# Kernel tuning notes

Hardware: AMD Instinct MI355X
Metric: run time of the kernel (lower is better)

Reference implementation:

```python
import jax, jax.numpy as jnp
import numpy as np

NUM_HEADS = 16

def rotate_half(x):
    x1, x2 = jnp.split(x, 2, axis=-1)
    return jnp.concatenate((-x2, x1), axis=-1)

def setup_inputs() -> dict:
    key = jax.random.key(0)
    ks = jax.random.split(key, 5)
    b, n, dim, hd = 2, 2048, 1024, 64
    return {
        "x": jax.random.normal(ks[0], (b, n, dim), dtype=jnp.float32),
        "Wqkv": jax.random.normal(ks[1], (3 * dim, dim), dtype=jnp.float32) * (dim ** -0.5),
        "Wproj": jax.random.normal(ks[2], (dim, dim), dtype=jnp.float32) * (dim ** -0.5),
        "bproj": jnp.zeros((dim,), dtype=jnp.float32),
        "sin": jax.random.normal(ks[3], (n, hd), dtype=jnp.float32),
        "cos": jax.random.normal(ks[4], (n, hd), dtype=jnp.float32),
    }

def reference(x, Wqkv, Wproj, bproj, sin, cos):
    b, n, dim = x.shape
    h = NUM_HEADS
    d = dim // h
    qkv = x @ Wqkv.T
    qkv = qkv.reshape(b, n, 3, h, d).transpose(2, 0, 3, 1, 4)
    q, k, v = qkv[0], qkv[1], qkv[2]
    # RoPE: sin/cos [n, d] broadcast over [b, h, n, d]
    q = q * cos + rotate_half(q) * sin
    k = k * cos + rotate_half(k) * sin
    # SDPA (non-causal, no dropout at eval)
    scale = d ** -0.5
    scores = jnp.einsum("bhnd,bhmd->bhnm", q, k) * scale
    attn = jax.nn.softmax(scores, axis=-1)
    out = jnp.einsum("bhnm,bhmd->bhnd", attn, v)
    # merge heads: [b, h, n, d] -> [b, n, h*d]
    out = out.transpose(0, 2, 1, 3).reshape(b, n, dim)
    return out @ Wproj.T + bproj
```

## Files before the change

kernel.cpp:

```cpp
#include <hip/hip_runtime.h>
#include <hip/hip_fp16.h>

typedef _Float16 f16;
typedef _Float16 half8 __attribute__((ext_vector_type(8)));
typedef _Float16 half4v __attribute__((ext_vector_type(4)));
typedef float f32x4 __attribute__((ext_vector_type(4)));

#define QSCALE 0.18033688011112042f
#define SHIFT2 17.312340490667560f

__device__ __forceinline__ void gload_lds16(const void* g, void* lds) {
  __builtin_amdgcn_global_load_lds(
      (__attribute__((address_space(1))) void*)g,
      (__attribute__((address_space(3))) void*)lds, 16, 0, 0);
}

__global__ __launch_bounds__(256) void cvt_all_kernel(
    const float* __restrict__ x, const float* __restrict__ wqkv,
    const float* __restrict__ wproj, f16* __restrict__ xh,
    f16* __restrict__ wqkvh, f16* __restrict__ wprojh) {
  int i = blockIdx.x * 256 + threadIdx.x;
  const float* src; f16* dst; int off;
  if (i < 1048576)      { src = x;     dst = xh;     off = i; }
  else if (i < 1835008) { src = wqkv;  dst = wqkvh;  off = i - 1048576; }
  else                  { src = wproj; dst = wprojh; off = i - 1835008; }
  float4 v = ((const float4*)src)[off];
  half4v o;
  o.x = (f16)v.x; o.y = (f16)v.y; o.z = (f16)v.z; o.w = (f16)v.w;
  ((half4v*)dst)[off] = o;
}

template<int EPI>
__global__ __launch_bounds__(256) void hgemm_kernel(
    const f16* __restrict__ A16, const f16* __restrict__ B, int K,
    const float* __restrict__ cosT, const float* __restrict__ sinT,
    f16* __restrict__ Qout, f16* __restrict__ Kout, f16* __restrict__ Vtout,
    const float* __restrict__ bias, float* __restrict__ Cout) {
  constexpr int BN = (EPI == 0) ? 128 : 64;
  constexpr int NJ = (EPI == 0) ? 4 : 2;
  __shared__ f16 As[2][128 * 32];
  __shared__ f16 Bs[2][BN * 32];
  const int tid = threadIdx.x;
  const int lane = tid & 63, w = tid >> 6;
  const int fr = lane & 15, fkg = lane >> 4;
  const int wm = (w >> 1) * 64;
  const int wn = (EPI == 0) ? (w & 1) * 64 : (w & 1) * 16;
  const long long rowBase = (long long)blockIdx.x * 128;
  const long long colBase = (long long)blockIdx.y * BN;

  f32x4 acc[4][NJ] = {};
  const f16* Ab = A16 + rowBase * K;
  const f16* Bb = B + colBase * K;

  const int srow = lane >> 2;
  const int kcol = ((lane & 3) ^ ((lane >> 3) & 3)) * 8;
  const int sw = (fkg ^ ((fr >> 1) & 3)) * 8;

  auto stage = [&](int buf, int k0) {
#pragma unroll
    for (int r = 0; r < 2; ++r) {
      int c = r * 4 + w;
      gload_lds16(Ab + (long long)(c * 16 + srow) * K + k0 + kcol, &As[buf][c * 512]);
    }
    if (EPI == 0) {
#pragma unroll
      for (int r = 0; r < 2; ++r) {
        int c = r * 4 + w;
        gload_lds16(Bb + (long long)(c * 16 + srow) * K + k0 + kcol, &Bs[buf][c * 512]);
      }
    } else {
      int c = w;
      gload_lds16(Bb + (long long)(c * 16 + srow) * K + k0 + kcol, &Bs[buf][c * 512]);
    }
  };

  const int NT = K >> 5;
  stage(0, 0);
  stage(1, 32);
  for (int t = 0; t < NT; ++t) {
    const int buf = t & 1;
    const int k0 = t << 5;
    if (t + 1 < NT) {
      if constexpr (EPI == 0) asm volatile("s_waitcnt vmcnt(4)" ::: "memory");
      else                    asm volatile("s_waitcnt vmcnt(3)" ::: "memory");
    } else {
      asm volatile("s_waitcnt vmcnt(0)" ::: "memory");
    }
    __builtin_amdgcn_s_barrier();
    __builtin_amdgcn_sched_barrier(0);
    half8 a[4], b[NJ];
#pragma unroll
    for (int i = 0; i < 4; ++i)
      a[i] = *(const half8*)(&As[buf][((wm >> 4) + i) * 512 + fr * 32 + sw]);
#pragma unroll
    for (int j = 0; j < NJ; ++j) {
      int chunk = (EPI == 0) ? ((wn >> 4) + j) : ((wn >> 4) + j * 2);
      b[j] = *(const half8*)(&Bs[buf][chunk * 512 + fr * 32 + sw]);
    }
    asm volatile("s_waitcnt lgkmcnt(0)" ::: "memory");
    __builtin_amdgcn_sched_barrier(0);
    __builtin_amdgcn_s_barrier();
    if (t + 2 < NT) stage(buf, k0 + 64);
#pragma unroll
    for (int i = 0; i < 4; ++i)
#pragma unroll
      for (int j = 0; j < NJ; ++j)
        acc[i][j] = __builtin_amdgcn_mfma_f32_16x16x32_f16(a[i], b[j], acc[i][j], 0, 0, 0);
  }

  if (EPI == 0) {
#pragma unroll
    for (int i = 0; i < 4; ++i) {
#pragma unroll
      for (int r = 0; r < 4; ++r) {
        int rg = (int)rowBase + wm + i * 16 + fkg * 4 + r;
        int bidx = rg >> 11, nn = rg & 2047;
#pragma unroll
        for (int j = 0; j < 4; ++j) {
          int cg = (int)colBase + wn + j * 16 + fr;
          int t = cg >> 10, cc = cg & 1023;
          int head = cc >> 6, d = cc & 63;
          int bh = bidx * 16 + head;
          float v = acc[i][j][r];
          if (t == 2) {
            Vtout[((long long)bh * 64 + d) * 2048 + nn] = (f16)v;
          } else {
            float pal = acc[i][j ^ 2][r];
            float cs = cosT[nn * 64 + d];
            float sn = sinT[nn * 64 + d];
            v = v * cs + (d < 32 ? -pal : pal) * sn;
            if (t == 0) v *= QSCALE;
            f16 hv = (f16)v;
            if (t == 0) Qout[((long long)bh * 2048 + nn) * 64 + d] = hv;
            else        Kout[((long long)bh * 2048 + nn) * 64 + d] = hv;
          }
        }
      }
    }
  } else {
#pragma unroll
    for (int i = 0; i < 4; ++i)
#pragma unroll
      for (int r = 0; r < 4; ++r) {
        long long rg = rowBase + wm + i * 16 + fkg * 4 + r;
#pragma unroll
        for (int j = 0; j < NJ; ++j) {
          int cg = (int)colBase + wn + j * 32 + fr;
          Cout[rg * 1024 + cg] = acc[i][j][r] + bias[cg];
        }
      }
  }
}

__global__ __launch_bounds__(256) void attn_kernel(
    const f16* __restrict__ Q, const f16* __restrict__ Kb,
    const f16* __restrict__ Vt, f16* __restrict__ Om) {
  __shared__ f16 Ks[2][64 * 64];
  __shared__ f16 Vs[2][64 * 64];
  const int tid = threadIdx.x;
  const int lane = tid & 63, w = tid >> 6;
  const int fr = lane & 15, fkg = lane >> 4, fk = fkg * 8;

  const int lin = blockIdx.x;
  const int slot = lin >> 3;
  const int bh = (lin & 7) * 4 + (slot >> 4);
  const int q0 = (slot & 15) * 128 + w * 32;

  const f16* Kbh = Kb + (long long)bh * 2048 * 64;
  const f16* Vbh = Vt + (long long)bh * 64 * 2048;

  half8 aq[2][2];
#pragma unroll
  for (int m = 0; m < 2; ++m)
#pragma unroll
    for (int ks = 0; ks < 2; ++ks)
      aq[m][ks] = *(const half8*)(Q + ((long long)bh * 2048 + q0 + m * 16 + fr) * 64 +
                                  ks * 32 + fk);

  half8 ones_frag;
#pragma unroll
  for (int j = 0; j < 8; ++j) ones_frag[j] = (fr == 0) ? (f16)1.0f : (f16)0.0f;

  f32x4 acc[2][4] = {};
  f32x4 accL[2] = {};

  const int srow = lane >> 3;
  const int ssub = ((lane & 7) ^ srow) * 8;
  int prow[2];
#pragma unroll
  for (int c = 0; c < 2; ++c) {
    int R = w * 16 + c * 8 + srow;
    prow[c] = (R & 0x23) | ((R & 0x0C) << 1) | ((R & 0x10) >> 2);
  }

  auto stage = [&](int buf, int kv0) {
#pragma unroll
    for (int c = 0; c < 2; ++c) {
      int rb = w * 16 + c * 8;
      gload_lds16(Kbh + (long long)(kv0 + prow[c]) * 64 + ssub,
                  &Ks[buf][rb * 64]);
      gload_lds16(Vbh + (long long)(rb + srow) * 2048 + kv0 + ssub,
                  &Vs[buf][rb * 64]);
    }
  };

  stage(0, 0);
  stage(1, 64);
  for (int t = 0; t < 32; ++t) {
    const int buf = t & 1;
    if (t + 1 < 32) asm volatile("s_waitcnt vmcnt(4)" ::: "memory");
    else            asm volatile("s_waitcnt vmcnt(0)" ::: "memory");
    __builtin_amdgcn_s_barrier();
    __builtin_amdgcn_sched_barrier(0);

    f32x4 z[2][4];
#pragma unroll
    for (int n = 0; n < 4; ++n) {
      half8 bk0 = *(const half8*)(&Ks[buf][(n * 16 + fr) * 64 + ((fkg ^ (fr & 7)) * 8)]);
      half8 bk1 = *(const half8*)(&Ks[buf][(n * 16 + fr) * 64 + (((4 | fkg) ^ (fr & 7)) * 8)]);
#pragma unroll
      for (int m = 0; m < 2; ++m) {
        f32x4 tz = {0.f, 0.f, 0.f, 0.f};
        tz = __builtin_amdgcn_mfma_f32_16x16x32_f16(bk0, aq[m][0], tz, 0, 0, 0);
        tz = __builtin_amdgcn_mfma_f32_16x16x32_f16(bk1, aq[m][1], tz, 0, 0, 0);
        z[m][n] = tz;
      }
    }

    half8 av[2][4];
#pragma unroll
    for (int ks = 0; ks < 2; ++ks)
#pragma unroll
      for (int dd = 0; dd < 4; ++dd)
        av[ks][dd] = *(const half8*)(&Vs[buf][(dd * 16 + fr) * 64 +
                                              ((((ks << 2) | fkg) ^ (fr & 7)) * 8)]);

    half8 ap[2][2];
#pragma unroll
    for (int m = 0; m < 2; ++m)
#pragma unroll
      for (int ks = 0; ks < 2; ++ks)
#pragma unroll
        for (int h = 0; h < 2; ++h)
#pragma unroll
          for (int r = 0; r < 4; ++r)
            ap[m][ks][h * 4 + r] =
                (f16)__builtin_amdgcn_exp2f(z[m][2 * ks + h][r] - SHIFT2);

#pragma unroll
    for (int ks = 0; ks < 2; ++ks) {
#pragma unroll
      for (int m = 0; m < 2; ++m)
        accL[m] = __builtin_amdgcn_mfma_f32_16x16x32_f16(ones_frag, ap[m][ks], accL[m], 0, 0, 0);
#pragma unroll
      for (int dd = 0; dd < 4; ++dd)
#pragma unroll
        for (int m = 0; m < 2; ++m)
          acc[m][dd] = __builtin_amdgcn_mfma_f32_16x16x32_f16(av[ks][dd], ap[m][ks], acc[m][dd], 0, 0, 0);
    }

    asm volatile("s_waitcnt lgkmcnt(0)" ::: "memory");
    __builtin_amdgcn_sched_barrier(0);
    __builtin_amdgcn_s_barrier();
    if (t + 2 < 32) stage(buf, (t + 2) * 64);
  }

  const int b = bh >> 4, h = bh & 15;
#pragma unroll
  for (int m = 0; m < 2; ++m) {
    float l = __shfl(accL[m][0], fr);
    float inv = 1.f / l;
#pragma unroll
    for (int dd = 0; dd < 4; ++dd) {
      half4v o;
#pragma unroll
      for (int r = 0; r < 4; ++r) o[r] = (f16)(acc[m][dd][r] * inv);
      *(half4v*)(&Om[((long long)b * 2048 + q0 + m * 16 + fr) * 1024 +
                     h * 64 + dd * 16 + fkg * 4]) = o;
    }
  }
}

extern "C" void kernel_launch(void* const* d_in, const int* in_sizes, int n_in,
                              void* d_out, int out_size, void* d_ws, size_t ws_size,
                              hipStream_t stream) {
  (void)in_sizes; (void)n_in; (void)out_size; (void)ws_size;
  const float* x     = (const float*)d_in[0];
  const float* Wqkv  = (const float*)d_in[1];
  const float* Wproj = (const float*)d_in[2];
  const float* bproj = (const float*)d_in[3];
  const float* sinT  = (const float*)d_in[4];
  const float* cosT  = (const float*)d_in[5];
  float* out = (float*)d_out;

  f16* ws     = (f16*)d_ws;
  f16* xh     = ws;
  f16* Om     = ws;
  f16* Wqkvh  = ws + 4194304;
  f16* Wprojh = ws + 7340032;
  f16* Qb     = ws + 8388608;
  f16* Kb     = ws + 12582912;
  f16* Vtb    = ws + 16777216;

  cvt_all_kernel<<<8192, 256, 0, stream>>>(x, Wqkv, Wproj, xh, Wqkvh, Wprojh);

  hgemm_kernel<0><<<dim3(32, 24), 256, 0, stream>>>(
      xh, Wqkvh, 1024, cosT, sinT, Qb, Kb, Vtb, nullptr, nullptr);

  attn_kernel<<<512, 256, 0, stream>>>(Qb, Kb, Vtb, Om);

  hgemm_kernel<1><<<dim3(32, 16), 256, 0, stream>>>(
      Om, Wprojh, 1024, nullptr, nullptr, nullptr, nullptr, nullptr, bproj, out);
}
```

Before: 125.9 us.

## Triple-buffer LDS staging in attention and half of QKV GEMM to drop a barrier

Adds a three-buffer LDS pipeline to the attention kernel and to a new GEMM variant. The next-next tile is prefetched right after the single per-iteration barrier, which removes the second barrier and the lgkmcnt wait at the end of each iteration. The QKV projection is now split into two launches over column halves, one using the old double-buffered path and one the new triple-buffered path, which looks like a side-by-side comparison. The cost is more LDS per block, which may lower occupancy, plus one extra kernel launch.

Result: slower. 159.4 us (+26.6%).

```diff
diff --git a/kernel.cpp b/kernel.cpp
--- a/kernel.cpp
+++ b/kernel.cpp
@@ -30,23 +30,24 @@
   ((half4v*)dst)[off] = o;
 }
 
-template<int EPI>
+template<int EPI, int VAR>
 __global__ __launch_bounds__(256) void hgemm_kernel(
-    const f16* __restrict__ A16, const f16* __restrict__ B, int K,
+    const f16* __restrict__ A16, const f16* __restrict__ B, int K, int yoff,
     const float* __restrict__ cosT, const float* __restrict__ sinT,
     f16* __restrict__ Qout, f16* __restrict__ Kout, f16* __restrict__ Vtout,
     const float* __restrict__ bias, float* __restrict__ Cout) {
   constexpr int BN = (EPI == 0) ? 128 : 64;
   constexpr int NJ = (EPI == 0) ? 4 : 2;
-  __shared__ f16 As[2][128 * 32];
-  __shared__ f16 Bs[2][BN * 32];
+  constexpr int NBUF = (VAR == 0) ? 2 : 3;
+  __shared__ f16 As[NBUF][128 * 32];
+  __shared__ f16 Bs[NBUF][BN * 32];
   const int tid = threadIdx.x;
   const int lane = tid & 63, w = tid >> 6;
   const int fr = lane & 15, fkg = lane >> 4;
   const int wm = (w >> 1) * 64;
   const int wn = (EPI == 0) ? (w & 1) * 64 : (w & 1) * 16;
   const long long rowBase = (long long)blockIdx.x * 128;
-  const long long colBase = (long long)blockIdx.y * BN;
+  const long long colBase = (long long)(blockIdx.y + yoff) * BN;
 
   f32x4 acc[4][NJ] = {};
   const f16* Ab = A16 + rowBase * K;
@@ -77,35 +78,66 @@
   const int NT = K >> 5;
   stage(0, 0);
   stage(1, 32);
-  for (int t = 0; t < NT; ++t) {
-    const int buf = t & 1;
-    const int k0 = t << 5;
-    if (t + 1 < NT) {
-      if constexpr (EPI == 0) asm volatile("s_waitcnt vmcnt(4)" ::: "memory");
-      else                    asm volatile("s_waitcnt vmcnt(3)" ::: "memory");
-    } else {
-      asm volatile("s_waitcnt vmcnt(0)" ::: "memory");
-    }
-    __builtin_amdgcn_s_barrier();
-    __builtin_amdgcn_sched_barrier(0);
-    half8 a[4], b[NJ];
-#pragma unroll
-    for (int i = 0; i < 4; ++i)
-      a[i] = *(const half8*)(&As[buf][((wm >> 4) + i) * 512 + fr * 32 + sw]);
-#pragma unroll
-    for (int j = 0; j < NJ; ++j) {
-      int chunk = (EPI == 0) ? ((wn >> 4) + j) : ((wn >> 4) + j * 2);
-      b[j] = *(const half8*)(&Bs[buf][chunk * 512 + fr * 32 + sw]);
-    }
-    asm volatile("s_waitcnt lgkmcnt(0)" ::: "memory");
-    __builtin_amdgcn_sched_barrier(0);
-    __builtin_amdgcn_s_barrier();
-    if (t + 2 < NT) stage(buf, k0 + 64);
-#pragma unroll
-    for (int i = 0; i < 4; ++i)
-#pragma unroll
-      for (int j = 0; j < NJ; ++j)
-        acc[i][j] = __builtin_amdgcn_mfma_f32_16x16x32_f16(a[i], b[j], acc[i][j], 0, 0, 0);
+  if (VAR == 0) {
+    for (int t = 0; t < NT; ++t) {
+      const int buf = t & 1;
+      const int k0 = t << 5;
+      if (t + 1 < NT) {
+        if constexpr (EPI == 0) asm volatile("s_waitcnt vmcnt(4)" ::: "memory");
+        else                    asm volatile("s_waitcnt vmcnt(3)" ::: "memory");
+      } else {
+        asm volatile("s_waitcnt vmcnt(0)" ::: "memory");
+      }
+      __builtin_amdgcn_s_barrier();
+      __builtin_amdgcn_sched_barrier(0);
+      half8 a[4], b[NJ];
+#pragma unroll
+      for (int i = 0; i < 4; ++i)
+        a[i] = *(const half8*)(&As[buf][((wm >> 4) + i) * 512 + fr * 32 + sw]);
+#pragma unroll
+      for (int j = 0; j < NJ; ++j) {
+        int chunk = (EPI == 0) ? ((wn >> 4) + j) : ((wn >> 4) + j * 2);
+        b[j] = *(const half8*)(&Bs[buf][chunk * 512 + fr * 32 + sw]);
+      }
+      asm volatile("s_waitcnt lgkmcnt(0)" ::: "memory");
+      __builtin_amdgcn_sched_barrier(0);
+      __builtin_amdgcn_s_barrier();
+      if (t + 2 < NT) stage(buf, k0 + 64);
+#pragma unroll
+      for (int i = 0; i < 4; ++i)
+#pragma unroll
+        for (int j = 0; j < NJ; ++j)
+          acc[i][j] = __builtin_amdgcn_mfma_f32_16x16x32_f16(a[i], b[j], acc[i][j], 0, 0, 0);
+    }
+  } else {
+    int bcur = 0, bst = 2;
+    for (int t = 0; t < NT; ++t) {
+      if (t + 1 < NT) {
+        if constexpr (EPI == 0) asm volatile("s_waitcnt vmcnt(4)" ::: "memory");
+        else                    asm volatile("s_waitcnt vmcnt(3)" ::: "memory");
+      } else {
+        asm volatile("s_waitcnt vmcnt(0)" ::: "memory");
+      }
+      __builtin_amdgcn_s_barrier();
+      __builtin_amdgcn_sched_barrier(0);
+      if (t + 2 < NT) stage(bst, (t + 2) << 5);
+      half8 a[4], b[NJ];
+#pragma unroll
+      for (int i = 0; i < 4; ++i)
+        a[i] = *(const half8*)(&As[bcur][((wm >> 4) + i) * 512 + fr * 32 + sw]);
+#pragma unroll
+      for (int j = 0; j < NJ; ++j) {
+        int chunk = (EPI == 0) ? ((wn >> 4) + j) : ((wn >> 4) + j * 2);
+        b[j] = *(const half8*)(&Bs[bcur][chunk * 512 + fr * 32 + sw]);
+      }
+#pragma unroll
+      for (int i = 0; i < 4; ++i)
+#pragma unroll
+        for (int j = 0; j < NJ; ++j)
+          acc[i][j] = __builtin_amdgcn_mfma_f32_16x16x32_f16(a[i], b[j], acc[i][j], 0, 0, 0);
+      bcur = (bcur == 2) ? 0 : bcur + 1;
+      bst  = (bst == 2) ? 0 : bst + 1;
+    }
   }
 
   if (EPI == 0) {
@@ -155,8 +187,8 @@
 __global__ __launch_bounds__(256) void attn_kernel(
     const f16* __restrict__ Q, const f16* __restrict__ Kb,
     const f16* __restrict__ Vt, f16* __restrict__ Om) {
-  __shared__ f16 Ks[2][64 * 64];
-  __shared__ f16 Vs[2][64 * 64];
+  __shared__ f16 Ks[3][64 * 64];
+  __shared__ f16 Vs[3][64 * 64];
   const int tid = threadIdx.x;
   const int lane = tid & 63, w = tid >> 6;
   const int fr = lane & 15, fkg = lane >> 4, fk = fkg * 8;
@@ -197,27 +229,26 @@
 #pragma unroll
     for (int c = 0; c < 2; ++c) {
       int rb = w * 16 + c * 8;
-      gload_lds16(Kbh + (long long)(kv0 + prow[c]) * 64 + ssub,
-                  &Ks[buf][rb * 64]);
-      gload_lds16(Vbh + (long long)(rb + srow) * 2048 + kv0 + ssub,
-                  &Vs[buf][rb * 64]);
+      gload_lds16(Kbh + (long long)(kv0 + prow[c]) * 64 + ssub, &Ks[buf][rb * 64]);
+      gload_lds16(Vbh + (long long)(rb + srow) * 2048 + kv0 + ssub, &Vs[buf][rb * 64]);
     }
   };
 
   stage(0, 0);
   stage(1, 64);
+  int bcur = 0, bst = 2;
   for (int t = 0; t < 32; ++t) {
-    const int buf = t & 1;
     if (t + 1 < 32) asm volatile("s_waitcnt vmcnt(4)" ::: "memory");
     else            asm volatile("s_waitcnt vmcnt(0)" ::: "memory");
     __builtin_amdgcn_s_barrier();
     __builtin_amdgcn_sched_barrier(0);
+    if (t + 2 < 32) stage(bst, (t + 2) * 64);
 
     f32x4 z[2][4];
 #pragma unroll
     for (int n = 0; n < 4; ++n) {
-      half8 bk0 = *(const half8*)(&Ks[buf][(n * 16 + fr) * 64 + ((fkg ^ (fr & 7)) * 8)]);
-      half8 bk1 = *(const half8*)(&Ks[buf][(n * 16 + fr) * 64 + (((4 | fkg) ^ (fr & 7)) * 8)]);
+      half8 bk0 = *(const half8*)(&Ks[bcur][(n * 16 + fr) * 64 + ((fkg ^ (fr & 7)) * 8)]);
+      half8 bk1 = *(const half8*)(&Ks[bcur][(n * 16 + fr) * 64 + (((4 | fkg) ^ (fr & 7)) * 8)]);
 #pragma unroll
       for (int m = 0; m < 2; ++m) {
         f32x4 tz = {0.f, 0.f, 0.f, 0.f};
@@ -232,8 +263,8 @@
     for (int ks = 0; ks < 2; ++ks)
 #pragma unroll
       for (int dd = 0; dd < 4; ++dd)
-        av[ks][dd] = *(const half8*)(&Vs[buf][(dd * 16 + fr) * 64 +
-                                              ((((ks << 2) | fkg) ^ (fr & 7)) * 8)]);
+        av[ks][dd] = *(const half8*)(&Vs[bcur][(dd * 16 + fr) * 64 +
+                                               ((((ks << 2) | fkg) ^ (fr & 7)) * 8)]);
 
     half8 ap[2][2];
 #pragma unroll
@@ -258,11 +289,8 @@
         for (int m = 0; m < 2; ++m)
           acc[m][dd] = __builtin_amdgcn_mfma_f32_16x16x32_f16(av[ks][dd], ap[m][ks], acc[m][dd], 0, 0, 0);
     }
-
-    asm volatile("s_waitcnt lgkmcnt(0)" ::: "memory");
-    __builtin_amdgcn_sched_barrier(0);
-    __builtin_amdgcn_s_barrier();
-    if (t + 2 < 32) stage(buf, (t + 2) * 64);
+    bcur = (bcur == 2) ? 0 : bcur + 1;
+    bst  = (bst == 2) ? 0 : bst + 1;
   }
 
   const int b = bh >> 4, h = bh & 15;
@@ -304,11 +332,13 @@
 
   cvt_all_kernel<<<8192, 256, 0, stream>>>(x, Wqkv, Wproj, xh, Wqkvh, Wprojh);
 
-  hgemm_kernel<0><<<dim3(32, 24), 256, 0, stream>>>(
-      xh, Wqkvh, 1024, cosT, sinT, Qb, Kb, Vtb, nullptr, nullptr);
+  hgemm_kernel<0, 0><<<dim3(32, 12), 256, 0, stream>>>(
+      xh, Wqkvh, 1024, 0, cosT, sinT, Qb, Kb, Vtb, nullptr, nullptr);
+  hgemm_kernel<0, 1><<<dim3(32, 12), 256, 0, stream>>>(
+      xh, Wqkvh, 1024, 12, cosT, sinT, Qb, Kb, Vtb, nullptr, nullptr);
 
   attn_kernel<<<512, 256, 0, stream>>>(Qb, Kb, Vtb, Om);
 
-  hgemm_kernel<1><<<dim3(32, 16), 256, 0, stream>>>(
-      Om, Wprojh, 1024, nullptr, nullptr, nullptr, nullptr, nullptr, bproj, out);
-}
+  hgemm_kernel<1, 0><<<dim3(32, 16), 256, 0, stream>>>(
+      Om, Wprojh, 1024, 0, nullptr, nullptr, nullptr, nullptr, nullptr, bproj, out);
+}
```
